# Performance work log

Measured on AMD Instinct MI355X. Metric: run time of the kernel, lower is better.

The kernel has to match this reference:

```python
import jax, jax.numpy as jnp
import numpy as np

TLAMBDA = 0.5
DELTA = 0.1
PROP_LAYERS = 2
LN_EPS = 1e-12
MASK_NEG = -10000.0
N_HEADS = 4


def _ln(x, g, b):
    m = x.mean(-1, keepdims=True)
    v = ((x - m) ** 2).mean(-1, keepdims=True)
    return (x - m) * jax.lax.rsqrt(v + LN_EPS) * g + b


def _l2norm(x):
    # F.normalize(p=2, dim=-1) with eps=1e-12
    n = jnp.sqrt((x * x).sum(-1, keepdims=True))
    return x / jnp.maximum(n, 1e-12)


def _sparse_prop(op):
    # op: [B, N, 2] rows of (col_idx, weight). result[b,j,m] = w_j*w_m if idx_j==idx_m else 0
    idx = op[..., 0].astype(jnp.int32)
    w = op[..., 1]
    eq = idx[:, :, None] == idx[:, None, :]
    return jnp.where(eq, w[:, :, None] * w[:, None, :], jnp.zeros((), op.dtype))


def _prop(t, P):
    enc = t
    for _ in range(PROP_LAYERS):
        t = jnp.einsum('bnm,bme->bne', P, t) + DELTA * enc
    return t


def _bert_layer(h, mask, Wq, bq, Wk, bk, Wv, bv, Wo, bo, g1, b1, Wi, bi, Wf, bf, g2, b2):
    AN, S, E = h.shape
    dh = E // N_HEADS

    def heads(x):
        return x.reshape(AN, S, N_HEADS, dh).transpose(0, 2, 1, 3)

    q = heads(h @ Wq + bq)
    k = heads(h @ Wk + bk)
    v = heads(h @ Wv + bv)
    scores = jnp.einsum('ahsd,ahtd->ahst', q, k) / np.float32(np.sqrt(dh)) + mask
    probs = jax.nn.softmax(scores, axis=-1)
    ctx = jnp.einsum('ahst,ahtd->ahsd', probs, v).transpose(0, 2, 1, 3).reshape(AN, S, E)
    a = _ln(ctx @ Wo + bo + h, g1, b1)
    f = jax.nn.gelu(a @ Wi + bi, approximate=False)
    return _ln(f @ Wf + bf + a, g2, b2)


def reference(token_edges_batch, hidden_states, attention_mask, query_embedding, key_embedding,
              user_operator, item_operator, distance_embedding, centrality_embedding,
              Wq, bq, Wk, bk, Wv, bv, Wo, bo, ln_att_g, ln_att_b, Wi, bi, Wf, bf, ln_ffn_g, ln_ffn_b,
              W_agg, b_agg, W_d1, b_d1, ln1_g, ln1_b, W_d2, b_d2, ln2_g, ln2_b):
    B, N, _ = token_edges_batch.shape
    AN, S, E = hidden_states.shape
    L = Wq.shape[0]

    U = _sparse_prop(user_operator)   # [B, N, N]
    I = _sparse_prop(item_operator)
    sub_next_q = jnp.zeros((B, N, E), hidden_states.dtype)
    sub_next_k = jnp.zeros((B, N, E), hidden_states.dtype)
    mask0 = attention_mask.at[..., :4].set(MASK_NEG)

    hs = hidden_states.reshape(B, N, S, E)
    all_hs = []
    for i in range(L):
        all_hs.append(hs)
        if i > 0:
            hs = (hs.at[:, :, 0].set(query_embedding)
                    .at[:, :, 1].set(key_embedding)
                    .at[:, :, 2].set(distance_embedding)
                    .at[:, :, 3].set(centrality_embedding))
        p1 = _ln(_prop(TLAMBDA * query_embedding + sub_next_q, U) @ W_d1 + b_d1, ln1_g, ln1_b)
        p2 = _ln(_prop(TLAMBDA * key_embedding + sub_next_k, I) @ W_d2 + b_d2, ln2_g, ln2_b)
        mask = mask0 if i == 0 else attention_mask
        h = _bert_layer(hs.reshape(AN, S, E), mask,
                        Wq[i], bq[i], Wk[i], bk[i], Wv[i], bv[i], Wo[i], bo[i],
                        ln_att_g[i], ln_att_b[i], Wi[i], bi[i], Wf[i], bf[i], ln_ffn_g[i], ln_ffn_b[i])
        hs = h.reshape(B, N, S, E)
        sub_next_q = hs[:, :, 0, :]
        sub_next_k = hs[:, :, 1, :]
        snt = _l2norm(hs[:, 0, 4, :])                       # [B, E]
        p = jnp.concatenate([snt, p1[:, 0, :], p2[:, 1, :]], axis=1)  # [B, 3E]
        agg = _l2norm(jax.nn.relu(p @ W_agg[i] + b_agg[i]))
        hs = hs.at[:, 0, 4, :].set(agg)
    all_hs.append(hs)

    out1 = all_hs[L - 1][:, 0, 4:, :].mean(axis=1)
    out2 = all_hs[L][:, 0, 4:, :].mean(axis=1)
    return 0.5 * (out1 + out2)


def setup_inputs() -> dict:
    key = jax.random.key(0)
    ks = jax.random.split(key, 40)
    B, N, S, E, L, FF = 64, 64, 32, 256, 2, 1024
    AN = B * N
    f = jnp.float32
    inp = {}
    inp['token_edges_batch'] = jax.random.randint(ks[0], (B, N, 8), 0, 100)
    inp['hidden_states'] = jax.random.normal(ks[1], (AN, S, E), f)
    inp['attention_mask'] = jnp.zeros((AN, 1, 1, S), f)
    inp['query_embedding'] = jax.random.normal(ks[2], (B, N, E), f)
    inp['key_embedding'] = jax.random.normal(ks[3], (B, N, E), f)
    inp['distance_embedding'] = jax.random.normal(ks[4], (B, N, E), f)
    inp['centrality_embedding'] = jax.random.normal(ks[5], (B, N, E), f)

    def make_op(k1, k2):
        idx = jax.random.randint(k1, (B, N), 0, 16).astype(f)
        w = jax.random.uniform(k2, (B, N), f)
        return jnp.stack([idx, w], axis=-1)

    inp['user_operator'] = make_op(ks[6], ks[7])
    inp['item_operator'] = make_op(ks[8], ks[9])

    sc = 0.02
    def w(k, shape):
        return jax.random.normal(k, shape, f) * sc

    inp['Wq'] = w(ks[10], (L, E, E)); inp['bq'] = jnp.zeros((L, E), f)
    inp['Wk'] = w(ks[11], (L, E, E)); inp['bk'] = jnp.zeros((L, E), f)
    inp['Wv'] = w(ks[12], (L, E, E)); inp['bv'] = jnp.zeros((L, E), f)
    inp['Wo'] = w(ks[13], (L, E, E)); inp['bo'] = jnp.zeros((L, E), f)
    inp['ln_att_g'] = jnp.ones((L, E), f); inp['ln_att_b'] = jnp.zeros((L, E), f)
    inp['Wi'] = w(ks[14], (L, E, FF)); inp['bi'] = jnp.zeros((L, FF), f)
    inp['Wf'] = w(ks[15], (L, FF, E)); inp['bf'] = jnp.zeros((L, E), f)
    inp['ln_ffn_g'] = jnp.ones((L, E), f); inp['ln_ffn_b'] = jnp.zeros((L, E), f)
    inp['W_agg'] = w(ks[16], (L, 3 * E, E)); inp['b_agg'] = jnp.zeros((L, E), f)
    inp['W_d1'] = w(ks[17], (E, E)); inp['b_d1'] = jnp.zeros((E,), f)
    inp['ln1_g'] = jnp.ones((E,), f); inp['ln1_b'] = jnp.zeros((E,), f)
    inp['W_d2'] = w(ks[18], (E, E)); inp['b_d2'] = jnp.zeros((E,), f)
    inp['ln2_g'] = jnp.ones((E,), f); inp['ln2_b'] = jnp.zeros((E,), f)
    return inp
```

## Files before the change

### kernel.cpp

```cpp
#include <hip/hip_runtime.h>
#include <math.h>

#define E 256
#define SEQ 32
#define FF 1024
#define NEG_MASK -10000.0f

typedef __attribute__((ext_vector_type(8))) short bf16x8;
typedef __attribute__((ext_vector_type(4))) short s16x4;
typedef __attribute__((ext_vector_type(4))) float f32x4;
typedef __attribute__((ext_vector_type(16))) float f32x16;

__device__ __forceinline__ float bf2f(unsigned short u) {
  unsigned v = ((unsigned)u) << 16; float f; __builtin_memcpy(&f, &v, 4); return f;
}
__device__ __forceinline__ unsigned short f2bf(float f) {
  unsigned u; __builtin_memcpy(&u, &f, 4);
  unsigned r = (u + 0x7fffu + ((u >> 16) & 1u)) >> 16;
  return (unsigned short)r;
}
__device__ __forceinline__ s16x4 f2bf4(float4 v) {
  s16x4 r;
  r[0] = (short)f2bf(v.x); r[1] = (short)f2bf(v.y);
  r[2] = (short)f2bf(v.z); r[3] = (short)f2bf(v.w);
  return r;
}
__device__ __forceinline__ f32x4 mfma16(bf16x8 a, bf16x8 b, f32x4 c) {
  return __builtin_amdgcn_mfma_f32_16x16x32_bf16(a, b, c, 0, 0, 0);
}
__device__ __forceinline__ f32x16 mfma32(bf16x8 a, bf16x8 b, f32x16 c) {
  return __builtin_amdgcn_mfma_f32_32x32x16_bf16(a, b, c, 0, 0, 0);
}
__device__ __forceinline__ float block_sum256(float v, float* tmp4) {
  #pragma unroll
  for (int o = 32; o > 0; o >>= 1) v += __shfl_down(v, o);
  int wid = threadIdx.x >> 6, lane = threadIdx.x & 63;
  if (lane == 0) tmp4[wid] = v;
  __syncthreads();
  float r = tmp4[0] + tmp4[1] + tmp4[2] + tmp4[3];
  __syncthreads();
  return r;
}

__global__ __launch_bounds__(256) void wprep_kernel(
    const float* __restrict__ Wq, const float* __restrict__ Wk,
    const float* __restrict__ Wv, const float* __restrict__ Wo,
    const float* __restrict__ Wi, const float* __restrict__ Wf,
    unsigned short* wqt, unsigned short* wkt, unsigned short* wvt,
    unsigned short* wot, unsigned short* wit, unsigned short* wft) {
  int type = blockIdx.y, ll = blockIdx.z, t = threadIdx.x;
  const float* src; unsigned short* dst; int Kd, Nd, m32;
  switch (type) {
    case 0: src = Wq + (size_t)ll * 65536;  dst = wqt + (size_t)ll * 65536;  Kd = 256;  Nd = 256;  m32 = 0; break;
    case 1: src = Wk + (size_t)ll * 65536;  dst = wkt + (size_t)ll * 65536;  Kd = 256;  Nd = 256;  m32 = 0; break;
    case 2: src = Wv + (size_t)ll * 65536;  dst = wvt + (size_t)ll * 65536;  Kd = 256;  Nd = 256;  m32 = 0; break;
    case 3: src = Wo + (size_t)ll * 65536;  dst = wot + (size_t)ll * 65536;  Kd = 256;  Nd = 256;  m32 = 0; break;
    case 4: src = Wi + (size_t)ll * 262144; dst = wit + (size_t)ll * 262144; Kd = 256;  Nd = 1024; m32 = 1; break;
    default: src = Wf + (size_t)ll * 262144; dst = wft + (size_t)ll * 262144; Kd = 1024; Nd = 256; m32 = 1; break;
  }
  int frag = blockIdx.x * 4 + (t >> 6);
  int l = t & 63;
  int nkc = m32 ? (Kd >> 4) : (Kd >> 5);
  int nfrag = (m32 ? (Nd >> 5) : (Nd >> 4)) * nkc;
  if (frag >= nfrag) return;
  int n, k0;
  if (m32) { n = (frag / nkc) * 32 + (l & 31); k0 = (frag % nkc) * 16 + (l >> 5) * 8; }
  else     { n = (frag / nkc) * 16 + (l & 15); k0 = (frag % nkc) * 32 + (l >> 4) * 8; }
  unsigned short vv[8];
  #pragma unroll
  for (int j = 0; j < 8; ++j) vv[j] = f2bf(src[(size_t)(k0 + j) * Nd + n]);
  unsigned short* o = dst + (size_t)frag * 512 + l * 8;
  #pragma unroll
  for (int j = 0; j < 8; ++j) o[j] = vv[j];
}

__global__ __launch_bounds__(256) void prop_ln_kernel(
    const float* __restrict__ emb_q, const float* __restrict__ emb_k,
    const float* snq,
    const float* __restrict__ uop, const float* __restrict__ iop,
    const float* __restrict__ Wd1, const float* __restrict__ bd1,
    const float* __restrict__ g1v, const float* __restrict__ b1v,
    const float* __restrict__ Wd2, const float* __restrict__ bd2,
    const float* __restrict__ g2v, const float* __restrict__ b2v,
    float* __restrict__ out1, float* __restrict__ out2) {
  int sel = blockIdx.y;
  const float* emb = sel ? emb_k : emb_q;
  const float* op  = sel ? iop : uop;
  const float* Wd  = sel ? Wd2 : Wd1;
  const float* bd  = sel ? bd2 : bd1;
  const float* g   = sel ? g2v : g1v;
  const float* bvec= sel ? b2v : b1v;
  float* outp      = sel ? out2 : out1;
  int row = sel;
  __shared__ float t0s[64][E];
  __shared__ float s1[16 * E];
  __shared__ float s2[16 * E];
  __shared__ float wv[64];
  __shared__ int gi[64];
  __shared__ float t2row[E];
  __shared__ float tmp4[4];
  int b = blockIdx.x, e = threadIdx.x;
  if (e < 64) {
    wv[e] = op[(b * 64 + e) * 2 + 1];
    gi[e] = (int)op[(b * 64 + e) * 2 + 0];
  }
  for (int gg = 0; gg < 16; ++gg) { s1[gg * E + e] = 0.f; s2[gg * E + e] = 0.f; }
  for (int n = 0; n < 64; ++n) {
    float t0 = 0.5f * emb[(size_t)(b * 64 + n) * E + e];
    if (snq) t0 += snq[((size_t)(b * 64 + n) * 2 + sel) * E + e];
    t0s[n][e] = t0;
  }
  __syncthreads();
  for (int n = 0; n < 64; ++n) s1[gi[n] * E + e] += wv[n] * t0s[n][e];
  for (int n = 0; n < 64; ++n) {
    float t1 = wv[n] * s1[gi[n] * E + e] + 0.1f * t0s[n][e];
    s2[gi[n] * E + e] += wv[n] * t1;
  }
  float t2 = wv[row] * s2[gi[row] * E + e] + 0.1f * t0s[row][e];
  t2row[e] = t2;
  __syncthreads();
  float y = bd[e];
  for (int k = 0; k < E; ++k) y = fmaf(t2row[k], Wd[k * E + e], y);
  float ssum = block_sum256(y, tmp4);
  float qsum = block_sum256(y * y, tmp4);
  float m = ssum * (1.f / E);
  float var = qsum * (1.f / E) - m * m;
  outp[b * E + e] = (y - m) * rsqrtf(var + 1e-12f) * g[e] + bvec[e];
}

__global__ __launch_bounds__(256, 4) void seq_attn_mfma(
    const float* __restrict__ hidden,
    const unsigned short* __restrict__ wqt, const float* __restrict__ bq,
    const unsigned short* __restrict__ wkt, const float* __restrict__ bk,
    const unsigned short* __restrict__ wvt, const float* __restrict__ bv,
    const float* __restrict__ mask, unsigned short* __restrict__ ctx_all,
    unsigned short* __restrict__ Kf, unsigned short* __restrict__ Vf) {
  __shared__ __align__(16) unsigned short aT[32][264];
  __shared__ __align__(16) unsigned short kvb[32][272];
  __shared__ __align__(16) unsigned short qs16[2][264];
  __shared__ float pr[4][2][36];
  int a = blockIdx.x, t = threadIdx.x;
  int w = t >> 6, l = t & 63;
  int lm = l & 15, lkq = l >> 4, lk = lkq << 3;
  size_t hb = (size_t)a * (SEQ * E);
  #pragma unroll
  for (int i = 0; i < 8; ++i) {
    int p = i * 256 + t; int row = p >> 6, c4 = (p & 63) << 2;
    float4 v = *(const float4*)&hidden[hb + row * E + c4];
    *(s16x4*)&aT[row][c4] = f2bf4(v);
  }
  __syncthreads();
  bool isn0 = ((a & 63) == 0);
  int nb = a >> 6;
  f32x4 zz = {0.f, 0.f, 0.f, 0.f};
  #pragma unroll
  for (int nt = 0; nt < 4; ++nt) {
    int ncol = w * 64 + nt * 16 + lm;
    const unsigned short* bkrow = wkt + ((size_t)(w * 4 + nt) * 8) * 512 + l * 8;
    const unsigned short* bqrow = wqt + ((size_t)(w * 4 + nt) * 8) * 512 + l * 8;
    bf16x8 bk8[8], bq8[8];
    #pragma unroll
    for (int kc = 0; kc < 8; ++kc) bk8[kc] = *(const bf16x8*)(bkrow + kc * 512);
    #pragma unroll
    for (int kc = 0; kc < 8; ++kc) bq8[kc] = *(const bf16x8*)(bqrow + kc * 512);
    f32x4 ak0 = zz, ak1 = zz, aq = zz;
    #pragma unroll
    for (int kc = 0; kc < 8; ++kc) {
      bf16x8 a0 = *(const bf16x8*)&aT[lm][kc * 32 + lk];
      bf16x8 a1 = *(const bf16x8*)&aT[16 + lm][kc * 32 + lk];
      ak0 = mfma16(a0, bk8[kc], ak0);
      ak1 = mfma16(a1, bk8[kc], ak1);
      aq  = mfma16(a0, bq8[kc], aq);
    }
    float bb = bk[ncol];
    #pragma unroll
    for (int r = 0; r < 4; ++r) {
      int rw = (lkq << 2) + r;
      float v0 = ak0[r] + bb, v1 = ak1[r] + bb;
      kvb[rw][ncol] = f2bf(v0);
      kvb[16 + rw][ncol] = f2bf(v1);
      if (isn0) {
        Kf[((size_t)nb * 32 + rw) * 256 + ncol] = f2bf(v0);
        Kf[((size_t)nb * 32 + 16 + rw) * 256 + ncol] = f2bf(v1);
      }
    }
    if (lkq == 0) {
      float bqv = bq[ncol];
      qs16[0][ncol] = f2bf(aq[0] + bqv);
      qs16[1][ncol] = f2bf(aq[1] + bqv);
    }
  }
  __syncthreads();
  {
    f32x4 sc0 = zz, sc1 = zz;
    #pragma unroll
    for (int kc2 = 0; kc2 < 2; ++kc2) {
      bf16x8 aq = *(const bf16x8*)&qs16[lm & 1][w * 64 + kc2 * 32 + lk];
      bf16x8 b0 = *(const bf16x8*)&kvb[lm][w * 64 + kc2 * 32 + lk];
      bf16x8 b1 = *(const bf16x8*)&kvb[16 + lm][w * 64 + kc2 * 32 + lk];
      sc0 = mfma16(aq, b0, sc0);
      sc1 = mfma16(aq, b1, sc1);
    }
    float mv0 = (lm < 4) ? NEG_MASK : mask[(size_t)a * SEQ + lm];
    float mv1 = mask[(size_t)a * SEQ + 16 + lm];
    #pragma unroll
    for (int r = 0; r < 2; ++r) {
      float s0 = sc0[r] * 0.125f + mv0;
      float s1 = sc1[r] * 0.125f + mv1;
      float mx = fmaxf(s0, s1);
      mx = fmaxf(mx, __shfl_xor(mx, 1));
      mx = fmaxf(mx, __shfl_xor(mx, 2));
      mx = fmaxf(mx, __shfl_xor(mx, 4));
      mx = fmaxf(mx, __shfl_xor(mx, 8));
      float e0 = expf(s0 - mx), e1 = expf(s1 - mx);
      float se = e0 + e1;
      se += __shfl_xor(se, 1); se += __shfl_xor(se, 2);
      se += __shfl_xor(se, 4); se += __shfl_xor(se, 8);
      float inv = 1.f / se;
      if (lkq == 0) {
        pr[w][r][lm] = e0 * inv;
        pr[w][r][16 + lm] = e1 * inv;
      }
    }
  }
  __syncthreads();
  #pragma unroll
  for (int nt = 0; nt < 4; ++nt) {
    int ncol = w * 64 + nt * 16 + lm;
    const unsigned short* bvrow = wvt + ((size_t)(w * 4 + nt) * 8) * 512 + l * 8;
    bf16x8 bv8[8];
    #pragma unroll
    for (int kc = 0; kc < 8; ++kc) bv8[kc] = *(const bf16x8*)(bvrow + kc * 512);
    f32x4 av0 = zz, av1 = zz;
    #pragma unroll
    for (int kc = 0; kc < 8; ++kc) {
      bf16x8 a0 = *(const bf16x8*)&aT[lm][kc * 32 + lk];
      bf16x8 a1 = *(const bf16x8*)&aT[16 + lm][kc * 32 + lk];
      av0 = mfma16(a0, bv8[kc], av0);
      av1 = mfma16(a1, bv8[kc], av1);
    }
    float bb = bv[ncol];
    #pragma unroll
    for (int r = 0; r < 4; ++r) {
      int rw = (lkq << 2) + r;
      float v0 = av0[r] + bb, v1 = av1[r] + bb;
      kvb[rw][ncol] = f2bf(v0);
      kvb[16 + rw][ncol] = f2bf(v1);
      if (isn0) {
        Vf[((size_t)nb * 32 + rw) * 256 + ncol] = f2bf(v0);
        Vf[((size_t)nb * 32 + 16 + rw) * 256 + ncol] = f2bf(v1);
      }
    }
  }
  __syncthreads();
  {
    float o0 = 0.f, o1 = 0.f;
    #pragma unroll
    for (int tt = 0; tt < 32; ++tt) {
      float vv = bf2f(kvb[tt][t]);
      o0 = fmaf(pr[w][0][tt], vv, o0);
      o1 = fmaf(pr[w][1][tt], vv, o1);
    }
    ctx_all[((size_t)a * 2 + 0) * E + t] = f2bf(o0);
    ctx_all[((size_t)a * 2 + 1) * E + t] = f2bf(o1);
  }
}

__global__ __launch_bounds__(256) void gemm_bias_kernel(
    const float* __restrict__ Af, const unsigned short* __restrict__ Bt,
    const float* __restrict__ bias, unsigned short* __restrict__ outb) {
  __shared__ __align__(16) unsigned short aT[32][264];
  int t = threadIdx.x, w = t >> 6, l = t & 63;
  int lm = l & 15, lkq = l >> 4, lk = lkq << 3;
  int row0 = blockIdx.x * 32;
  #pragma unroll
  for (int i = 0; i < 8; ++i) {
    int p = i * 256 + t; int row = p >> 6, c4 = (p & 63) << 2;
    int gr = row0 + row;
    int src = ((gr >> 5) << 11) + (gr & 31);
    float4 v = *(const float4*)&Af[(size_t)src * E + c4];
    *(s16x4*)&aT[row][c4] = f2bf4(v);
  }
  __syncthreads();
  f32x4 zz = {0.f, 0.f, 0.f, 0.f};
  #pragma unroll
  for (int nt = 0; nt < 4; ++nt) {
    int ncol = w * 64 + nt * 16 + lm;
    const unsigned short* brow = Bt + ((size_t)(w * 4 + nt) * 8) * 512 + l * 8;
    bf16x8 b8[8];
    #pragma unroll
    for (int kc = 0; kc < 8; ++kc) b8[kc] = *(const bf16x8*)(brow + kc * 512);
    f32x4 c0 = zz, c1 = zz;
    #pragma unroll
    for (int kc = 0; kc < 8; ++kc) {
      bf16x8 a0 = *(const bf16x8*)&aT[lm][kc * 32 + lk];
      bf16x8 a1 = *(const bf16x8*)&aT[16 + lm][kc * 32 + lk];
      c0 = mfma16(a0, b8[kc], c0);
      c1 = mfma16(a1, b8[kc], c1);
    }
    float bb = bias[ncol];
    #pragma unroll
    for (int r = 0; r < 4; ++r) {
      int rw = (lkq << 2) + r;
      outb[(size_t)(row0 + rw) * E + ncol] = f2bf(c0[r] + bb);
      outb[(size_t)(row0 + 16 + rw) * E + ncol] = f2bf(c1[r] + bb);
    }
  }
}

__global__ __launch_bounds__(256) void qkv1_kernel(
    const unsigned short* __restrict__ Ab,
    const unsigned short* __restrict__ wq, const float* __restrict__ bqv,
    const unsigned short* __restrict__ wk, const float* __restrict__ bkv,
    const unsigned short* __restrict__ wv, const float* __restrict__ bvv,
    unsigned short* q2, unsigned short* k2, unsigned short* v2) {
  __shared__ __align__(16) unsigned short aT[32][264];
  int t = threadIdx.x, w = t >> 6, l = t & 63;
  int lm = l & 15, lkq = l >> 4, lk = lkq << 3;
  int row0 = blockIdx.x * 32;
  int m = blockIdx.y;
  const unsigned short* Wt = (m == 0) ? wq : (m == 1) ? wk : wv;
  const float* bb = (m == 0) ? bqv : (m == 1) ? bkv : bvv;
  unsigned short* outb = (m == 0) ? q2 : (m == 1) ? k2 : v2;
  #pragma unroll
  for (int i = 0; i < 4; ++i) {
    int p = i * 256 + t; int row = p >> 5, c8 = (p & 31) << 3;
    *(s16x4*)&aT[row][c8] = *(const s16x4*)&Ab[(size_t)(row0 + row) * E + c8];
    *(s16x4*)&aT[row][c8 + 4] = *(const s16x4*)&Ab[(size_t)(row0 + row) * E + c8 + 4];
  }
  __syncthreads();
  f32x4 zz = {0.f, 0.f, 0.f, 0.f};
  #pragma unroll
  for (int nt = 0; nt < 4; ++nt) {
    int ncol = w * 64 + nt * 16 + lm;
    const unsigned short* brow = Wt + ((size_t)(w * 4 + nt) * 8) * 512 + l * 8;
    bf16x8 b8[8];
    #pragma unroll
    for (int kc = 0; kc < 8; ++kc) b8[kc] = *(const bf16x8*)(brow + kc * 512);
    f32x4 c0 = zz, c1 = zz;
    #pragma unroll
    for (int kc = 0; kc < 8; ++kc) {
      bf16x8 a0 = *(const bf16x8*)&aT[lm][kc * 32 + lk];
      bf16x8 a1 = *(const bf16x8*)&aT[16 + lm][kc * 32 + lk];
      c0 = mfma16(a0, b8[kc], c0);
      c1 = mfma16(a1, b8[kc], c1);
    }
    float bv2 = bb[ncol];
    #pragma unroll
    for (int r = 0; r < 4; ++r) {
      int rw = (lkq << 2) + r;
      outb[(size_t)(row0 + rw) * E + ncol] = f2bf(c0[r] + bv2);
      outb[(size_t)(row0 + 16 + rw) * E + ncol] = f2bf(c1[r] + bv2);
    }
  }
}

__global__ __launch_bounds__(256) void attnf_kernel(
    const unsigned short* __restrict__ Q, const unsigned short* __restrict__ K,
    const unsigned short* __restrict__ V, unsigned short* __restrict__ CTX,
    const float* __restrict__ mask, int set4) {
  int b = blockIdx.x, h = blockIdx.y, t = threadIdx.x;
  __shared__ float qsh[32][65], ksh[32][65], vsh[32][65];
  __shared__ float pr[32][33];
  size_t base = (size_t)b * (SEQ * E) + h * 64;
  for (int i = 0; i < 8; ++i) {
    int p = i * 256 + t; int s = p >> 6, d = p & 63;
    qsh[s][d] = bf2f(Q[base + s * E + d]);
    ksh[s][d] = bf2f(K[base + s * E + d]);
    vsh[s][d] = bf2f(V[base + s * E + d]);
  }
  __syncthreads();
  for (int i = 0; i < 4; ++i) {
    int p = i * 256 + t; int s = p >> 5, tt = p & 31;
    float acc = 0.f;
    #pragma unroll
    for (int d = 0; d < 64; ++d) acc = fmaf(qsh[s][d], ksh[tt][d], acc);
    float mv = mask[(size_t)b * 2048 + tt];
    if (set4 && tt < 4) mv = NEG_MASK;
    pr[s][tt] = acc * 0.125f + mv;
  }
  __syncthreads();
  int rrow = t >> 3, l8 = t & 7;
  float vals[4];
  float mx = -1e30f;
  #pragma unroll
  for (int ii = 0; ii < 4; ++ii) { vals[ii] = pr[rrow][l8 + ii * 8]; mx = fmaxf(mx, vals[ii]); }
  mx = fmaxf(mx, __shfl_xor(mx, 1));
  mx = fmaxf(mx, __shfl_xor(mx, 2));
  mx = fmaxf(mx, __shfl_xor(mx, 4));
  float se = 0.f;
  #pragma unroll
  for (int ii = 0; ii < 4; ++ii) { vals[ii] = expf(vals[ii] - mx); se += vals[ii]; }
  se += __shfl_xor(se, 1); se += __shfl_xor(se, 2); se += __shfl_xor(se, 4);
  float inv = 1.f / se;
  #pragma unroll
  for (int ii = 0; ii < 4; ++ii) pr[rrow][l8 + ii * 8] = vals[ii] * inv;
  __syncthreads();
  for (int i = 0; i < 8; ++i) {
    int p = i * 256 + t; int s = p >> 6, d = p & 63;
    float acc = 0.f;
    #pragma unroll
    for (int tt = 0; tt < SEQ; ++tt) acc = fmaf(pr[s][tt], vsh[tt][d], acc);
    CTX[base + s * E + d] = f2bf(acc);
  }
}

__device__ __forceinline__ int map_res(int gr) {
  if (gr < 8192) return ((gr >> 1) << 5) + (gr & 1);
  int rr = gr - 8192;
  return ((rr >> 5) << 11) + (rr & 31);
}

__global__ __launch_bounds__(256) void tailA_mfma(
    const unsigned short* __restrict__ ctx,
    const unsigned short* __restrict__ wo, const float* __restrict__ bo,
    const float* __restrict__ Res, int resmode,
    const float* __restrict__ g1, const float* __restrict__ b1,
    unsigned short* __restrict__ a_bf, float* __restrict__ a_f32) {
  __shared__ __align__(16) unsigned short aT[32][264];
  __shared__ float sT[32][257];
  __shared__ float prs[32][4], prq[32][4];
  int t = threadIdx.x, w = t >> 6, l = t & 63;
  int row0 = blockIdx.x * 32;
  #pragma unroll
  for (int i = 0; i < 8; ++i) {
    int p = i * 256 + t; int row = p >> 6, c4 = (p & 63) << 2;
    *(s16x4*)&aT[row][c4] = *(const s16x4*)&ctx[(size_t)(row0 + row) * E + c4];
  }
  __syncthreads();
  {
    int lm = l & 15, lkq = l >> 4, lk = lkq << 3;
    f32x4 zz = {0.f, 0.f, 0.f, 0.f};
    #pragma unroll
    for (int nt = 0; nt < 4; ++nt) {
      int ncol = w * 64 + nt * 16 + lm;
      const unsigned short* brow = wo + ((size_t)(w * 4 + nt) * 8) * 512 + l * 8;
      bf16x8 b8[8];
      #pragma unroll
      for (int kc = 0; kc < 8; ++kc) b8[kc] = *(const bf16x8*)(brow + kc * 512);
      f32x4 c0 = zz, c1 = zz;
      #pragma unroll
      for (int kc = 0; kc < 8; ++kc) {
        bf16x8 a0 = *(const bf16x8*)&aT[lm][kc * 32 + lk];
        bf16x8 a1 = *(const bf16x8*)&aT[16 + lm][kc * 32 + lk];
        c0 = mfma16(a0, b8[kc], c0);
        c1 = mfma16(a1, b8[kc], c1);
      }
      float bb = bo[ncol];
      #pragma unroll
      for (int r = 0; r < 4; ++r) {
        int rw = (lkq << 2) + r;
        int rr0 = resmode ? map_res(row0 + rw) : (row0 + rw);
        int rr1 = resmode ? map_res(row0 + 16 + rw) : (row0 + 16 + rw);
        sT[rw][ncol] = c0[r] + bb + Res[(size_t)rr0 * E + ncol];
        sT[16 + rw][ncol] = c1[r] + bb + Res[(size_t)rr1 * E + ncol];
      }
    }
  }
  __syncthreads();
  {
    int wid = t >> 6, lane = t & 63;
    float vcache[32];
    for (int r = 0; r < 32; ++r) {
      float v = sT[r][t];
      vcache[r] = v;
      float s = v, q = v * v;
      #pragma unroll
      for (int o = 32; o > 0; o >>= 1) { s += __shfl_down(s, o); q += __shfl_down(q, o); }
      if (lane == 0) { prs[r][wid] = s; prq[r][wid] = q; }
    }
    __syncthreads();
    #pragma unroll
    for (int r = 0; r < 32; ++r) {
      float Sv = prs[r][0] + prs[r][1] + prs[r][2] + prs[r][3];
      float Qv = prq[r][0] + prq[r][1] + prq[r][2] + prq[r][3];
      float m = Sv * (1.f / E), var = Qv * (1.f / E) - m * m;
      float val = (vcache[r] - m) * rsqrtf(var + 1e-12f) * g1[t] + b1[t];
      a_f32[(size_t)(row0 + r) * E + t] = val;
      a_bf[(size_t)(row0 + r) * E + t] = f2bf(val);
    }
  }
}

__global__ __launch_bounds__(512) void ffnB_kernel(
    const unsigned short* __restrict__ a_bf,
    const unsigned short* __restrict__ wi, const float* __restrict__ bi,
    const unsigned short* __restrict__ wf,
    float* __restrict__ part, size_t pstride) {
  __shared__ __align__(16) unsigned short aT[32][264];
  __shared__ __align__(16) unsigned short fT[32][264];
  int t = threadIdx.x, w = t >> 6, l = t & 63;
  int lm = l & 31, lk = (l >> 5) << 3;
  int row0 = blockIdx.x * 32, qh = blockIdx.y;
  #pragma unroll
  for (int i = 0; i < 2; ++i) {
    int chunk = i * 512 + t; int row = chunk >> 5, c8 = (chunk & 31) << 3;
    *(s16x4*)&aT[row][c8] = *(const s16x4*)&a_bf[(size_t)(row0 + row) * E + c8];
    *(s16x4*)&aT[row][c8 + 4] = *(const s16x4*)&a_bf[(size_t)(row0 + row) * E + c8 + 4];
  }
  __syncthreads();
  f32x16 zz16 = {0};
  {
    const unsigned short* brow = wi + ((size_t)(qh * 8 + w) * 16) * 512 + l * 8;
    bf16x8 b16[16];
    #pragma unroll
    for (int kc = 0; kc < 16; ++kc) b16[kc] = *(const bf16x8*)(brow + kc * 512);
    f32x16 c = zz16;
    #pragma unroll
    for (int kc = 0; kc < 16; ++kc) {
      bf16x8 a = *(const bf16x8*)&aT[lm][kc * 16 + lk];
      c = mfma32(a, b16[kc], c);
    }
    int lcol = w * 32 + lm;
    float bib = bi[qh * 256 + lcol];
    #pragma unroll
    for (int reg = 0; reg < 16; ++reg) {
      int row = (reg & 3) + 8 * (reg >> 2) + 4 * (l >> 5);
      float x = c[reg] + bib;
      fT[row][lcol] = f2bf(0.5f * x * (1.f + erff(x * 0.70710678118654752f)));
    }
  }
  __syncthreads();
  {
    const unsigned short* brow = wf + ((size_t)(w * 64 + qh * 16)) * 512 + l * 8;
    bf16x8 b16[16];
    #pragma unroll
    for (int kc = 0; kc < 16; ++kc) b16[kc] = *(const bf16x8*)(brow + kc * 512);
    f32x16 c = zz16;
    #pragma unroll
    for (int kc = 0; kc < 16; ++kc) {
      bf16x8 a = *(const bf16x8*)&fT[lm][kc * 16 + lk];
      c = mfma32(a, b16[kc], c);
    }
    float* po = part + (size_t)qh * pstride;
    int col = w * 32 + lm;
    #pragma unroll
    for (int reg = 0; reg < 16; ++reg) {
      int row = (reg & 3) + 8 * (reg >> 2) + 4 * (l >> 5);
      po[(size_t)(row0 + row) * E + col] = c[reg];
    }
  }
}

__global__ __launch_bounds__(256) void ffnC_kernel(
    const float* __restrict__ part, size_t pstride,
    const float* __restrict__ bfv, const float* __restrict__ a_f32,
    const float* __restrict__ g2, const float* __restrict__ b2,
    float* __restrict__ out0, float* __restrict__ out1, int split) {
  __shared__ float prs[32][4], prq[32][4];
  int t = threadIdx.x;
  int row0 = blockIdx.x * 32;
  int wid = t >> 6, lane = t & 63;
  float bb = bfv[t];
  float vcache[32];
  for (int r = 0; r < 32; ++r) {
    size_t idx = (size_t)(row0 + r) * E + t;
    float v = part[idx] + part[pstride + idx] + part[2 * pstride + idx] +
              part[3 * pstride + idx] + bb + a_f32[idx];
    vcache[r] = v;
    float s = v, q = v * v;
    #pragma unroll
    for (int o = 32; o > 0; o >>= 1) { s += __shfl_down(s, o); q += __shfl_down(q, o); }
    if (lane == 0) { prs[r][wid] = s; prq[r][wid] = q; }
  }
  __syncthreads();
  #pragma unroll
  for (int r = 0; r < 32; ++r) {
    float Sv = prs[r][0] + prs[r][1] + prs[r][2] + prs[r][3];
    float Qv = prq[r][0] + prq[r][1] + prq[r][2] + prq[r][3];
    float m = Sv * (1.f / E), var = Qv * (1.f / E) - m * m;
    float val = (vcache[r] - m) * rsqrtf(var + 1e-12f) * g2[t] + b2[t];
    int gr = row0 + r;
    if (gr < split) out0[(size_t)gr * E + t] = val;
    else            out1[(size_t)(gr - split) * E + t] = val;
  }
}

__global__ __launch_bounds__(256) void agg_build_kernel(
    const float* __restrict__ h1n0,
    const float* __restrict__ p1, const float* __restrict__ p2,
    const float* __restrict__ Wagg, const float* __restrict__ bagg,
    const float* __restrict__ qe, const float* __restrict__ ke,
    const float* __restrict__ de, const float* __restrict__ ce,
    float* __restrict__ agg0,
    float* __restrict__ h2f, unsigned short* __restrict__ h2b) {
  __shared__ float pv[768];
  __shared__ float tmp4[4];
  int b = blockIdx.x, t = threadIdx.x;
  float x = h1n0[(size_t)b * (SEQ * E) + 4 * E + t];
  float n2 = block_sum256(x * x, tmp4);
  pv[t] = x / fmaxf(sqrtf(n2), 1e-12f);
  pv[256 + t] = p1[b * E + t];
  pv[512 + t] = p2[b * E + t];
  __syncthreads();
  float y = bagg[t];
  for (int u = 0; u < 768; ++u) y = fmaf(pv[u], Wagg[u * E + t], y);
  y = fmaxf(y, 0.f);
  float n3 = block_sum256(y * y, tmp4);
  float aggv = y / fmaxf(sqrtf(n3), 1e-12f);
  agg0[b * E + t] = aggv;
  size_t eb = (size_t)(b * 64) * E + t;
  size_t ob = (size_t)b * (SEQ * E);
  float v;
  v = qe[eb];  h2f[ob + 0 * E + t] = v; h2b[ob + 0 * E + t] = f2bf(v);
  v = ke[eb];  h2f[ob + 1 * E + t] = v; h2b[ob + 1 * E + t] = f2bf(v);
  v = de[eb];  h2f[ob + 2 * E + t] = v; h2b[ob + 2 * E + t] = f2bf(v);
  v = ce[eb];  h2f[ob + 3 * E + t] = v; h2b[ob + 3 * E + t] = f2bf(v);
  h2f[ob + 4 * E + t] = aggv; h2b[ob + 4 * E + t] = f2bf(aggv);
  for (int s = 5; s < SEQ; ++s) {
    v = h1n0[ob + s * E + t];
    h2f[ob + s * E + t] = v; h2b[ob + s * E + t] = f2bf(v);
  }
}

__global__ __launch_bounds__(256) void agg_kernel(
    const float* __restrict__ hbase,
    const float* __restrict__ p1, const float* __restrict__ p2,
    const float* __restrict__ Wagg, const float* __restrict__ bagg,
    float* __restrict__ outp) {
  __shared__ float pv[768];
  __shared__ float tmp4[4];
  int b = blockIdx.x, t = threadIdx.x;
  float x = hbase[(size_t)b * (SEQ * E) + 4 * E + t];
  float n2 = block_sum256(x * x, tmp4);
  pv[t] = x / fmaxf(sqrtf(n2), 1e-12f);
  pv[256 + t] = p1[b * E + t];
  pv[512 + t] = p2[b * E + t];
  __syncthreads();
  float y = bagg[t];
  for (int u = 0; u < 768; ++u) y = fmaf(pv[u], Wagg[u * E + t], y);
  y = fmaxf(y, 0.f);
  float n3 = block_sum256(y * y, tmp4);
  outp[b * E + t] = y / fmaxf(sqrtf(n3), 1e-12f);
}

__global__ __launch_bounds__(256) void out_kernel(
    const float* __restrict__ h1n0, const float* __restrict__ agg0,
    const float* __restrict__ h2, const float* __restrict__ agg1,
    float* __restrict__ outp) {
  int b = blockIdx.x, t = threadIdx.x;
  size_t ob = (size_t)b * (SEQ * E);
  float s1v = agg0[b * E + t];
  float s2v = agg1[b * E + t];
  for (int s = 5; s < SEQ; ++s) { s1v += h1n0[ob + s * E + t]; s2v += h2[ob + s * E + t]; }
  outp[b * E + t] = 0.5f * (s1v + s2v) * (1.f / 28.f);
}

extern "C" void kernel_launch(void* const* d_in, const int* in_sizes, int n_in,
                              void* d_out, int out_size, void* d_ws, size_t ws_size,
                              hipStream_t stream) {
  (void)in_sizes; (void)n_in; (void)out_size;
  const float* hidden = (const float*)d_in[1];
  const float* amask  = (const float*)d_in[2];
  const float* qemb   = (const float*)d_in[3];
  const float* kemb   = (const float*)d_in[4];
  const float* demb   = (const float*)d_in[5];
  const float* cemb   = (const float*)d_in[6];
  const float* uop    = (const float*)d_in[7];
  const float* iop    = (const float*)d_in[8];
  const float* Wq = (const float*)d_in[9];  const float* bq = (const float*)d_in[10];
  const float* Wk = (const float*)d_in[11]; const float* bk = (const float*)d_in[12];
  const float* Wv = (const float*)d_in[13]; const float* bv = (const float*)d_in[14];
  const float* Wo = (const float*)d_in[15]; const float* bo = (const float*)d_in[16];
  const float* g1 = (const float*)d_in[17]; const float* b1 = (const float*)d_in[18];
  const float* Wi = (const float*)d_in[19]; const float* bi = (const float*)d_in[20];
  const float* Wf = (const float*)d_in[21]; const float* bf = (const float*)d_in[22];
  const float* g2 = (const float*)d_in[23]; const float* b2 = (const float*)d_in[24];
  const float* Wagg = (const float*)d_in[25]; const float* bagg = (const float*)d_in[26];
  const float* Wd1 = (const float*)d_in[27]; const float* bd1 = (const float*)d_in[28];
  const float* l1g = (const float*)d_in[29]; const float* l1b = (const float*)d_in[30];
  const float* Wd2 = (const float*)d_in[31]; const float* bd2 = (const float*)d_in[32];
  const float* l2g = (const float*)d_in[33]; const float* l2b = (const float*)d_in[34];

  char* cur = (char*)d_ws;
  auto alloc_us = [&](size_t n) { unsigned short* p = (unsigned short*)cur; cur += ((n * 2 + 255) & ~(size_t)255); return p; };
  auto alloc_f  = [&](size_t n) { float* p = (float*)cur; cur += ((n * 4 + 255) & ~(size_t)255); return p; };
  unsigned short* wqt = alloc_us(131072);
  unsigned short* wkt = alloc_us(131072);
  unsigned short* wvt = alloc_us(131072);
  unsigned short* wot = alloc_us(131072);
  unsigned short* wit = alloc_us(524288);
  unsigned short* wft = alloc_us(524288);
  unsigned short* ctx_all = alloc_us((size_t)10240 * 256);
  unsigned short* qn0 = alloc_us((size_t)2048 * 256);
  unsigned short* Kf  = alloc_us((size_t)2048 * 256);
  unsigned short* Vf  = alloc_us((size_t)2048 * 256);
  unsigned short* h2inb = alloc_us((size_t)2048 * 256);
  unsigned short* a_bf = alloc_us((size_t)10240 * 256);
  unsigned short* q2b = alloc_us((size_t)2048 * 256);
  unsigned short* k2b = alloc_us((size_t)2048 * 256);
  unsigned short* v2b = alloc_us((size_t)2048 * 256);
  unsigned short* ctx1 = alloc_us((size_t)2048 * 256);
  float* a_f32 = alloc_f((size_t)10240 * 256);
  float* part  = alloc_f((size_t)4 * 10240 * 256);
  float* h101  = alloc_f((size_t)4096 * 2 * 256);
  float* h1n0  = alloc_f((size_t)2048 * 256);
  float* h2inf = alloc_f((size_t)2048 * 256);
  float* h2    = alloc_f((size_t)2048 * 256);
  float* p1_0  = alloc_f(64 * 256);
  float* p2_0  = alloc_f(64 * 256);
  float* p1_1  = alloc_f(64 * 256);
  float* p2_1  = alloc_f(64 * 256);
  float* agg0  = alloc_f(64 * 256);
  float* agg1  = alloc_f(64 * 256);
  if ((size_t)(cur - (char*)d_ws) > ws_size) return;
  const size_t PSTRIDE = (size_t)10240 * 256;

  wprep_kernel<<<dim3(128, 6, 2), 256, 0, stream>>>(Wq, Wk, Wv, Wo, Wi, Wf,
                                                    wqt, wkt, wvt, wot, wit, wft);

  prop_ln_kernel<<<dim3(64, 2), 256, 0, stream>>>(qemb, kemb, nullptr, uop, iop,
                                                  Wd1, bd1, l1g, l1b, Wd2, bd2, l2g, l2b,
                                                  p1_0, p2_0);
  seq_attn_mfma<<<4096, 256, 0, stream>>>(hidden, wqt, bq, wkt, bk, wvt, bv,
                                          amask, ctx_all, Kf, Vf);
  gemm_bias_kernel<<<64, 256, 0, stream>>>(hidden, wqt, bq, qn0);
  attnf_kernel<<<dim3(64, 4), 256, 0, stream>>>(qn0, Kf, Vf, ctx_all + (size_t)8192 * 256,
                                                amask, 1);
  tailA_mfma<<<320, 256, 0, stream>>>(ctx_all, wot, bo, hidden, 1, g1, b1, a_bf, a_f32);
  ffnB_kernel<<<dim3(320, 4), 512, 0, stream>>>(a_bf, wit, bi, wft, part, PSTRIDE);
  ffnC_kernel<<<320, 256, 0, stream>>>(part, PSTRIDE, bf, a_f32, g2, b2,
                                       h101, h1n0, 8192);
  agg_build_kernel<<<64, 256, 0, stream>>>(h1n0, p1_0, p2_0, Wagg, bagg,
                                           qemb, kemb, demb, cemb, agg0, h2inf, h2inb);

  prop_ln_kernel<<<dim3(64, 2), 256, 0, stream>>>(qemb, kemb, h101, uop, iop,
                                                  Wd1, bd1, l1g, l1b, Wd2, bd2, l2g, l2b,
                                                  p1_1, p2_1);
  qkv1_kernel<<<dim3(64, 3), 256, 0, stream>>>(h2inb,
                                               wqt + 65536, bq + E,
                                               wkt + 65536, bk + E,
                                               wvt + 65536, bv + E,
                                               q2b, k2b, v2b);
  attnf_kernel<<<dim3(64, 4), 256, 0, stream>>>(q2b, k2b, v2b, ctx1, amask, 0);
  tailA_mfma<<<64, 256, 0, stream>>>(ctx1, wot + 65536, bo + E, h2inf, 0,
                                     g1 + E, b1 + E, a_bf, a_f32);
  ffnB_kernel<<<dim3(64, 4), 512, 0, stream>>>(a_bf, wit + 262144, bi + FF,
                                               wft + 262144, part, PSTRIDE);
  ffnC_kernel<<<64, 256, 0, stream>>>(part, PSTRIDE, bf + E, a_f32,
                                      g2 + E, b2 + E, h2, h2, 1 << 30);
  agg_kernel<<<64, 256, 0, stream>>>(h2, p1_1, p2_1,
                                     Wagg + (size_t)768 * E, bagg + E, agg1);

  out_kernel<<<64, 256, 0, stream>>>(h1n0, agg0, h2, agg1, (float*)d_out);
}
```

Measured before the change: 386.7 us.

## Store FFN split-K partials in bf16, shrink prop LDS, fuse agg and output kernels

The FFN split-K partial sums are now written and read as bf16 instead of fp32, halving the traffic through the large partial buffer between ffnB and ffnC. The propagation kernel drops its 64xE shared-memory staging array and reloads the embeddings from global memory instead, cutting LDS use. The final aggregation and output kernels are merged into one launch. The bf16 partials lose some precision before the residual and layernorm.

```diff
diff --git a/kernel.cpp b/kernel.cpp
--- a/kernel.cpp
+++ b/kernel.cpp
@@ -92,7 +92,6 @@
   const float* bvec= sel ? b2v : b1v;
   float* outp      = sel ? out2 : out1;
   int row = sel;
-  __shared__ float t0s[64][E];
   __shared__ float s1[16 * E];
   __shared__ float s2[16 * E];
   __shared__ float wv[64];
@@ -105,18 +104,21 @@
     gi[e] = (int)op[(b * 64 + e) * 2 + 0];
   }
   for (int gg = 0; gg < 16; ++gg) { s1[gg * E + e] = 0.f; s2[gg * E + e] = 0.f; }
+  __syncthreads();
+  float t0r = 0.f;
   for (int n = 0; n < 64; ++n) {
     float t0 = 0.5f * emb[(size_t)(b * 64 + n) * E + e];
     if (snq) t0 += snq[((size_t)(b * 64 + n) * 2 + sel) * E + e];
-    t0s[n][e] = t0;
-  }
-  __syncthreads();
-  for (int n = 0; n < 64; ++n) s1[gi[n] * E + e] += wv[n] * t0s[n][e];
+    if (n == row) t0r = t0;
+    s1[gi[n] * E + e] += wv[n] * t0;
+  }
   for (int n = 0; n < 64; ++n) {
-    float t1 = wv[n] * s1[gi[n] * E + e] + 0.1f * t0s[n][e];
+    float t0 = 0.5f * emb[(size_t)(b * 64 + n) * E + e];
+    if (snq) t0 += snq[((size_t)(b * 64 + n) * 2 + sel) * E + e];
+    float t1 = wv[n] * s1[gi[n] * E + e] + 0.1f * t0;
     s2[gi[n] * E + e] += wv[n] * t1;
   }
-  float t2 = wv[row] * s2[gi[row] * E + e] + 0.1f * t0s[row][e];
+  float t2 = wv[row] * s2[gi[row] * E + e] + 0.1f * t0r;
   t2row[e] = t2;
   __syncthreads();
   float y = bd[e];
@@ -486,7 +488,7 @@
     const unsigned short* __restrict__ a_bf,
     const unsigned short* __restrict__ wi, const float* __restrict__ bi,
     const unsigned short* __restrict__ wf,
-    float* __restrict__ part, size_t pstride) {
+    unsigned short* __restrict__ part, size_t pstride) {
   __shared__ __align__(16) unsigned short aT[32][264];
   __shared__ __align__(16) unsigned short fT[32][264];
   int t = threadIdx.x, w = t >> 6, l = t & 63;
@@ -532,18 +534,18 @@
       bf16x8 a = *(const bf16x8*)&fT[lm][kc * 16 + lk];
       c = mfma32(a, b16[kc], c);
     }
-    float* po = part + (size_t)qh * pstride;
+    unsigned short* po = part + (size_t)qh * pstride;
     int col = w * 32 + lm;
     #pragma unroll
     for (int reg = 0; reg < 16; ++reg) {
       int row = (reg & 3) + 8 * (reg >> 2) + 4 * (l >> 5);
-      po[(size_t)(row0 + row) * E + col] = c[reg];
+      po[(size_t)(row0 + row) * E + col] = f2bf(c[reg]);
     }
   }
 }
 
 __global__ __launch_bounds__(256) void ffnC_kernel(
-    const float* __restrict__ part, size_t pstride,
+    const unsigned short* __restrict__ part, size_t pstride,
     const float* __restrict__ bfv, const float* __restrict__ a_f32,
     const float* __restrict__ g2, const float* __restrict__ b2,
     float* __restrict__ out0, float* __restrict__ out1, int split) {
@@ -555,8 +557,9 @@
   float vcache[32];
   for (int r = 0; r < 32; ++r) {
     size_t idx = (size_t)(row0 + r) * E + t;
-    float v = part[idx] + part[pstride + idx] + part[2 * pstride + idx] +
-              part[3 * pstride + idx] + bb + a_f32[idx];
+    float v = bf2f(part[idx]) + bf2f(part[pstride + idx]) +
+              bf2f(part[2 * pstride + idx]) + bf2f(part[3 * pstride + idx]) +
+              bb + a_f32[idx];
     vcache[r] = v;
     float s = v, q = v * v;
     #pragma unroll
@@ -613,15 +616,16 @@
   }
 }
 
-__global__ __launch_bounds__(256) void agg_kernel(
-    const float* __restrict__ hbase,
+__global__ __launch_bounds__(256) void agg_out_kernel(
+    const float* __restrict__ h2,
     const float* __restrict__ p1, const float* __restrict__ p2,
     const float* __restrict__ Wagg, const float* __restrict__ bagg,
+    const float* __restrict__ h1n0, const float* __restrict__ agg0,
     float* __restrict__ outp) {
   __shared__ float pv[768];
   __shared__ float tmp4[4];
   int b = blockIdx.x, t = threadIdx.x;
-  float x = hbase[(size_t)b * (SEQ * E) + 4 * E + t];
+  float x = h2[(size_t)b * (SEQ * E) + 4 * E + t];
   float n2 = block_sum256(x * x, tmp4);
   pv[t] = x / fmaxf(sqrtf(n2), 1e-12f);
   pv[256 + t] = p1[b * E + t];
@@ -631,17 +635,10 @@
   for (int u = 0; u < 768; ++u) y = fmaf(pv[u], Wagg[u * E + t], y);
   y = fmaxf(y, 0.f);
   float n3 = block_sum256(y * y, tmp4);
-  outp[b * E + t] = y / fmaxf(sqrtf(n3), 1e-12f);
-}
-
-__global__ __launch_bounds__(256) void out_kernel(
-    const float* __restrict__ h1n0, const float* __restrict__ agg0,
-    const float* __restrict__ h2, const float* __restrict__ agg1,
-    float* __restrict__ outp) {
-  int b = blockIdx.x, t = threadIdx.x;
+  float agg1v = y / fmaxf(sqrtf(n3), 1e-12f);
   size_t ob = (size_t)b * (SEQ * E);
   float s1v = agg0[b * E + t];
-  float s2v = agg1[b * E + t];
+  float s2v = agg1v;
   for (int s = 5; s < SEQ; ++s) { s1v += h1n0[ob + s * E + t]; s2v += h2[ob + s * E + t]; }
   outp[b * E + t] = 0.5f * (s1v + s2v) * (1.f / 28.f);
 }
@@ -691,8 +688,8 @@
   unsigned short* k2b = alloc_us((size_t)2048 * 256);
   unsigned short* v2b = alloc_us((size_t)2048 * 256);
   unsigned short* ctx1 = alloc_us((size_t)2048 * 256);
+  unsigned short* part = alloc_us((size_t)4 * 10240 * 256);
   float* a_f32 = alloc_f((size_t)10240 * 256);
-  float* part  = alloc_f((size_t)4 * 10240 * 256);
   float* h101  = alloc_f((size_t)4096 * 2 * 256);
   float* h1n0  = alloc_f((size_t)2048 * 256);
   float* h2inf = alloc_f((size_t)2048 * 256);
@@ -702,7 +699,6 @@
   float* p1_1  = alloc_f(64 * 256);
   float* p2_1  = alloc_f(64 * 256);
   float* agg0  = alloc_f(64 * 256);
-  float* agg1  = alloc_f(64 * 256);
   if ((size_t)(cur - (char*)d_ws) > ws_size) return;
   const size_t PSTRIDE = (size_t)10240 * 256;
 
@@ -739,8 +735,7 @@
                                                wft + 262144, part, PSTRIDE);
   ffnC_kernel<<<64, 256, 0, stream>>>(part, PSTRIDE, bf + E, a_f32,
                                       g2 + E, b2 + E, h2, h2, 1 << 30);
-  agg_kernel<<<64, 256, 0, stream>>>(h2, p1_1, p2_1,
-                                     Wagg + (size_t)768 * E, bagg + E, agg1);
-
-  out_kernel<<<64, 256, 0, stream>>>(h1n0, agg0, h2, agg1, (float*)d_out);
-}
+  agg_out_kernel<<<64, 256, 0, stream>>>(h2, p1_1, p2_1,
+                                         Wagg + (size_t)768 * E, bagg + E,
+                                         h1n0, agg0, (float*)d_out);
+}
```

After: 382.8 us, median of 2. About the same (-1.0%).
